# Optimization experiments

Measured on AMD Instinct MI355X. Metric: run time of the kernel, lower is better.

The kernel has to match this reference:

```python
import jax, jax.numpy as jnp
import numpy as np

H = 768      # hidden_size
NH = 12      # num_attention_heads
HD = H // NH # head_dim = 64
EPS = 1e-5


def setup_inputs() -> dict:
    key = jax.random.key(0)
    ks = jax.random.split(key, 12)
    B, S = 2, 2048
    s = 1.0 / np.sqrt(H)
    return {
        "hidden_states": jax.random.normal(ks[0], (B, S, H), dtype=jnp.float32),
        "attention_mask": jax.random.normal(ks[1], (B, S), dtype=jnp.float32),
        "Wq": jax.random.normal(ks[2], (H, H), dtype=jnp.float32) * s,
        "bq": jnp.zeros((H,), dtype=jnp.float32),
        "Wk": jax.random.normal(ks[3], (H, H), dtype=jnp.float32) * s,
        "bk": jnp.zeros((H,), dtype=jnp.float32),
        "Wv": jax.random.normal(ks[4], (H, H), dtype=jnp.float32) * s,
        "bv": jnp.zeros((H,), dtype=jnp.float32),
        "Wo": jax.random.normal(ks[5], (H, H), dtype=jnp.float32) * s,
        "bo": jnp.zeros((H,), dtype=jnp.float32),
        "ln_gamma": jnp.ones((H,), dtype=jnp.float32),
        "ln_beta": jnp.zeros((H,), dtype=jnp.float32),
    }


def reference(hidden_states, attention_mask, Wq, bq, Wk, bk, Wv, bv, Wo, bo, ln_gamma, ln_beta):
    B, S, E = hidden_states.shape
    # QKV projections -> [B, NH, S, HD]
    def proj(W, b):
        return (hidden_states @ W + b).reshape(B, S, NH, HD).transpose(0, 2, 1, 3)
    q = proj(Wq, bq)
    k = proj(Wk, bk)
    v = proj(Wv, bv)
    # scores [B, NH, S, S]
    att = jnp.einsum('bhqd,bhkd->bhqk', q, k) * (1.0 / np.sqrt(HD))
    # padding pair mask: valid iff mask>=0 at both query and key positions
    valid = (attention_mask >= 0)  # [B, S]
    pair = valid[:, None, :, None] & valid[:, None, None, :]  # [B,1,S,S]
    att = jnp.where(pair, att, -1e9)
    att = jax.nn.softmax(att, axis=-1)
    # dropout p=0 (eval) -> identity
    ctx = jnp.einsum('bhqk,bhkd->bhqd', att, v)  # [B,NH,S,HD]
    ctx = ctx.transpose(0, 2, 1, 3).reshape(B, S, E)
    # output dense + residual + LayerNorm
    h = ctx @ Wo + bo + hidden_states
    mu = jnp.mean(h, axis=-1, keepdims=True)
    var = jnp.mean(jnp.square(h - mu), axis=-1, keepdims=True)
    out = (h - mu) * jax.lax.rsqrt(var + EPS) * ln_gamma + ln_beta
    return out
```

## Files before the change

kernel.cpp:

```cpp
#include <hip/hip_runtime.h>
#include <hip/hip_bf16.h>

#define H_DIM 768
#define NHEAD 12
#define HDIM  64
#define S_LEN 2048
#define B_SZ  2
#define M_TOT (B_SZ * S_LEN)
#define NQKV  (3 * H_DIM)
#define LN_EPS 1e-5f
#define SM_C   0.1803368801f

typedef __attribute__((ext_vector_type(8)))  short bf16x8;
typedef __attribute__((ext_vector_type(4)))  float f32x4;
typedef __attribute__((ext_vector_type(16))) float f32x16;
typedef __attribute__((ext_vector_type(4)))  int   i32x4;

static __device__ inline ushort f2bf(float x) {
    __hip_bfloat16 h = __float2bfloat16(x);
    ushort u;
    __builtin_memcpy(&u, &h, 2);
    return u;
}
static __device__ inline float bf2f(ushort u) {
    unsigned int v = ((unsigned int)u) << 16;
    float f;
    __builtin_memcpy(&f, &v, 4);
    return f;
}
static __device__ inline unsigned cvt_pk_bf16(float lo, float hi) {
    unsigned r;
    asm("v_cvt_pk_bf16_f32 %0, %1, %2" : "=v"(r) : "v"(lo), "v"(hi));
    return r;
}

#define GLDS16(g, l) __builtin_amdgcn_global_load_lds( \
    (const __attribute__((address_space(1))) void*)(g), \
    (__attribute__((address_space(3))) void*)(l), 16, 0, 0)

__global__ __launch_bounds__(256)
void prep(const float* __restrict__ hs,
          const float* __restrict__ Wq, const float* __restrict__ Wk,
          const float* __restrict__ Wv, const float* __restrict__ Wo,
          const float* __restrict__ bq, const float* __restrict__ bk,
          const float* __restrict__ bv,
          ushort* __restrict__ Xbf, ushort* __restrict__ Wcat,
          ushort* __restrict__ Wot, float* __restrict__ bcat)
{
    __shared__ ushort T[64][65];
    const int bid = blockIdx.x;
    const int t   = threadIdx.x;

    if (bid < 3072) {
        const int i = (bid * 256 + t) * 4;
        f32x4 v = *(const f32x4*)(hs + i);
        ushort4 o;
        o.x = f2bf(v[0]); o.y = f2bf(v[1]); o.z = f2bf(v[2]); o.w = f2bf(v[3]);
        *(ushort4*)(Xbf + i) = o;
    } else if (bid < 3072 + 576) {
        const int bid2 = bid - 3072;
        const int z = bid2 / 144;
        const int rem = bid2 % 144;
        const int n0 = (rem / 12) * 64;
        const int k0 = (rem % 12) * 64;
        const float* W = (z == 0) ? Wq : (z == 1) ? Wk : (z == 2) ? Wv : Wo;
        const int r = t >> 2, c0 = (t & 3) * 16;
        const float* src = W + (size_t)(k0 + r) * H_DIM + n0 + c0;
        #pragma unroll
        for (int j = 0; j < 16; j += 4) {
            f32x4 v = *(const f32x4*)(src + j);
            #pragma unroll
            for (int jj = 0; jj < 4; ++jj) T[r][c0 + j + jj] = f2bf(v[jj]);
        }
        __syncthreads();
        bf16x8 o0, o1;
        #pragma unroll
        for (int j = 0; j < 8; ++j) {
            o0[j] = (short)T[c0 + j][r];
            o1[j] = (short)T[c0 + 8 + j][r];
        }
        ushort* dst = (z < 3)
            ? Wcat + (size_t)(z * 768 + n0 + r) * H_DIM + k0 + c0
            : Wot  + (size_t)(n0 + r) * H_DIM + k0 + c0;
        *(bf16x8*)dst       = o0;
        *(bf16x8*)(dst + 8) = o1;
    } else {
        const int i = (bid - 3648) * 256 + t;
        if (i < NQKV) {
            float v = (i < 768) ? bq[i] : (i < 1536) ? bk[i - 768] : bv[i - 1536];
            bcat[i] = v;
        }
    }
}

template<int OUTMODE>
__global__ __launch_bounds__(256)
void gemm_mfma(const ushort* __restrict__ A, const ushort* __restrict__ Bt,
               const float* __restrict__ bias, const float* __restrict__ resid,
               void* __restrict__ outp, ushort* __restrict__ vtp,
               int M, int N, int K, int nscale, float sfac)
{
    __shared__ ushort As[128 * 32];
    __shared__ ushort Bs[128 * 32];
    const int bn = blockIdx.x * 128;
    const int bm = blockIdx.y * 128;
    const int t  = threadIdx.x;
    const int w  = t >> 6, l = t & 63;
    const int lg = l >> 4, lr = l & 15;
    const int wr = w >> 1, wc = w & 1;

    f32x4 acc[4][4];
    #pragma unroll
    for (int i = 0; i < 4; ++i)
        #pragma unroll
        for (int j = 0; j < 4; ++j) acc[i][j] = (f32x4){0.f, 0.f, 0.f, 0.f};

    for (int k0 = 0; k0 < K; k0 += 32) {
        #pragma unroll
        for (int it = 0; it < 2; ++it) {
            const int g = it * 256 + t;
            const int r = g >> 2, cb = (g & 3) * 8;
            GLDS16(A  + (size_t)(bm + r) * K + k0 + cb, (char*)As + g * 16);
            GLDS16(Bt + (size_t)(bn + r) * K + k0 + cb, (char*)Bs + g * 16);
        }
        __syncthreads();
        bf16x8 af[4], bfr[4];
        #pragma unroll
        for (int m16 = 0; m16 < 4; ++m16)
            af[m16] = *(const bf16x8*)&As[(wr * 64 + m16 * 16 + lr) * 32 + lg * 8];
        #pragma unroll
        for (int n16 = 0; n16 < 4; ++n16)
            bfr[n16] = *(const bf16x8*)&Bs[(wc * 64 + n16 * 16 + lr) * 32 + lg * 8];
        #pragma unroll
        for (int m16 = 0; m16 < 4; ++m16)
            #pragma unroll
            for (int n16 = 0; n16 < 4; ++n16)
                acc[m16][n16] = __builtin_amdgcn_mfma_f32_16x16x32_bf16(
                    af[m16], bfr[n16], acc[m16][n16], 0, 0, 0);
        __syncthreads();
    }

    #pragma unroll
    for (int m16 = 0; m16 < 4; ++m16) {
        #pragma unroll
        for (int n16 = 0; n16 < 4; ++n16) {
            const int col = bn + wc * 64 + n16 * 16 + lr;
            const float bcol = bias[col];
            const int row0 = bm + wr * 64 + m16 * 16 + lg * 4;
            float vv[4];
            #pragma unroll
            for (int r = 0; r < 4; ++r) {
                float v = acc[m16][n16][r] + bcol;
                if (OUTMODE == 1) v += resid[(size_t)(row0 + r) * N + col];
                else if (col < nscale) v *= sfac;
                vv[r] = v;
            }
            if (OUTMODE == 1) {
                #pragma unroll
                for (int r = 0; r < 4; ++r)
                    ((float*)outp)[(size_t)(row0 + r) * N + col] = vv[r];
            } else if (col >= 1536) {
                const int dfull = col - 1536;
                const int hh = dfull >> 6, dd = dfull & 63;
                const int bb = row0 >> 11, ss = row0 & 2047;
                ushort4 pk;
                pk.x = f2bf(vv[0]); pk.y = f2bf(vv[1]);
                pk.z = f2bf(vv[2]); pk.w = f2bf(vv[3]);
                *(ushort4*)(vtp + ((size_t)(bb * NHEAD + hh) * HDIM + dd) * S_LEN + ss) = pk;
            } else {
                #pragma unroll
                for (int r = 0; r < 4; ++r)
                    ((ushort*)outp)[(size_t)(row0 + r) * N + col] = f2bf(vv[r]);
            }
        }
    }
}

#define KT     64
#define ATT_QT 128
#define KVHALF (S_LEN / 2)
#define NTILES (KVHALF / KT)
#define KMSTR  (KVHALF + 4)

__global__ __launch_bounds__(256, 3)
void attn_mfma(const ushort* __restrict__ Qbf, const ushort* __restrict__ Kbf,
               const ushort* __restrict__ Vt, const float* __restrict__ mask,
               ushort* __restrict__ Pp, float* __restrict__ lp)
{
    const int flat = blockIdx.x;
    const int wk   = (flat & 7) * 96 + (flat >> 3);
    const int qt   = wk & 15;
    const int c_   = wk >> 4;
    const int h    = c_ % 12;
    const int bz   = c_ / 12;
    const int b    = bz >> 1, half = bz & 1;

    const int t  = threadIdx.x;
    const int w  = t >> 6, l = t & 63;
    const int l31 = l & 31, hi = l >> 5;
    const int q0 = qt * ATT_QT;
    const int kb0 = half * KVHALF;

    __shared__ ushort Ks[3][KT][64];
    __shared__ ushort Vs[2][HDIM][64];
    __shared__ float  kmarg[2 * KMSTR];

    {
        const int i = t * 4;
        f32x4 v = *(const f32x4*)(mask + b * S_LEN + kb0 + i);
        f32x4 o;
        #pragma unroll
        for (int j = 0; j < 4; ++j)
            o[j] = (v[j] >= 0.f) ? 0.f : -1e30f;
        *(f32x4*)&kmarg[i] = o;
        *(f32x4*)&kmarg[KMSTR + i] = o;
    }

    const bool qnL = (mask[b * S_LEN + q0 + w * 32 + l31] < 0.f);

    bf16x8 qa[4];
    {
        const ushort* qsrc = Qbf + (size_t)(b * S_LEN + q0 + w * 32 + l31) * NQKV
                           + h * HDIM + 8 * hi;
        #pragma unroll
        for (int k = 0; k < 4; ++k)
            qa[k] = *(const bf16x8*)(qsrc + 16 * k);
    }

    const int u    = l >> 3;
    const int scol = ((l & 7) ^ u) * 8;
    const int srcK = w * 16 + u + ((u & 4) ? 4 : 0);
    const int srow = w * 16 + u;
    const ushort* kLane = Kbf + (size_t)(b * S_LEN + kb0 + srcK) * NQKV
                        + h * HDIM + scol;
    const ushort* vLane = Vt + ((size_t)(b * NHEAD + h) * HDIM + srow) * S_LEN
                        + kb0 + scol;
    char* ldsK = (char*)Ks + w * 2048 + l * 16;
    char* ldsV = (char*)Vs + w * 2048 + l * 16;

    __syncthreads();

    GLDS16(kLane, ldsK);
    GLDS16(kLane + (size_t)4 * NQKV, ldsK + 1024);
    GLDS16(vLane, ldsV);
    GLDS16(vLane + (size_t)8 * S_LEN, ldsV + 1024);
    GLDS16(kLane + (size_t)KT * NQKV, ldsK + 8192);
    GLDS16(kLane + (size_t)(KT + 4) * NQKV, ldsK + 8192 + 1024);

    float l_part = 0.f;
    f32x16 accO[2];
    #pragma unroll
    for (int dt = 0; dt < 2; ++dt)
        #pragma unroll
        for (int i = 0; i < 16; ++i) accO[dt][i] = 0.f;

    const int swzl = (l31 & 7) << 4;
    const float* kmBase = &kmarg[hi * KMSTR];

    for (int tt = 0; tt < NTILES; ++tt) {
        if (tt < NTILES - 1) {
            asm volatile("s_waitcnt vmcnt(2)" ::: "memory");
        } else {
            asm volatile("s_waitcnt vmcnt(0)" ::: "memory");
        }
        __builtin_amdgcn_s_barrier();

        if (tt + 1 < NTILES) {
            const ushort* vsrc = vLane + (size_t)(tt + 1) * KT;
            char* lv = ldsV + ((tt + 1) & 1) * 8192;
            GLDS16(vsrc, lv);
            GLDS16(vsrc + (size_t)8 * S_LEN, lv + 1024);
            if (tt + 2 < NTILES) {
                const ushort* ksrc = kLane + (size_t)(tt + 2) * KT * NQKV;
                char* lk = ldsK + ((tt + 2) % 3) * 8192;
                GLDS16(ksrc, lk);
                GLDS16(ksrc + (size_t)4 * NQKV, lk + 1024);
            }
        }

        const char* Kc = (const char*)Ks + (tt % 3) * 8192;
        const char* Vc = (const char*)Vs + (tt & 1) * 8192;

        #pragma unroll
        for (int kvt = 0; kvt < 2; ++kvt) {
            f32x16 sc;
            __builtin_amdgcn_s_setprio(1);
            {
                const char* abase = Kc + (kvt * 32 + l31) * 128;
                bf16x8 a0 = *(const bf16x8*)(abase + ((16 * hi +  0) ^ swzl));
                bf16x8 a1 = *(const bf16x8*)(abase + ((16 * hi + 32) ^ swzl));
                bf16x8 a2 = *(const bf16x8*)(abase + ((16 * hi + 64) ^ swzl));
                bf16x8 a3 = *(const bf16x8*)(abase + ((16 * hi + 96) ^ swzl));
                f32x16 z;
                #pragma unroll
                for (int i = 0; i < 16; ++i) z[i] = 0.f;
                sc = __builtin_amdgcn_mfma_f32_32x32x16_bf16(a0, qa[0], z, 0, 0, 0);
                sc = __builtin_amdgcn_mfma_f32_32x32x16_bf16(a1, qa[1], sc, 0, 0, 0);
                sc = __builtin_amdgcn_mfma_f32_32x32x16_bf16(a2, qa[2], sc, 0, 0, 0);
                sc = __builtin_amdgcn_mfma_f32_32x32x16_bf16(a3, qa[3], sc, 0, 0, 0);
            }
            __builtin_amdgcn_s_setprio(0);

            float p[16];
            const float* km = kmBase + tt * 64 + kvt * 32;
            #pragma unroll
            for (int q4 = 0; q4 < 4; ++q4) {
                const int kvb = 16 * (q4 >> 1) + 8 * hi + 4 * (q4 & 1);
                f32x4 kq = *(const f32x4*)(km + kvb);
                #pragma unroll
                for (int r = 0; r < 4; ++r) {
                    float arg = sc[q4 * 4 + r] + kq[r];
                    arg = qnL ? 0.f : arg;
                    const float pv = exp2f(arg);
                    p[q4 * 4 + r] = pv;
                    l_part += pv;
                }
            }

            __builtin_amdgcn_s_setprio(1);
            #pragma unroll
            for (int cc = 0; cc < 2; ++cc) {
                i32x4 pku;
                pku[0] = (int)cvt_pk_bf16(p[8 * cc + 0], p[8 * cc + 1]);
                pku[1] = (int)cvt_pk_bf16(p[8 * cc + 2], p[8 * cc + 3]);
                pku[2] = (int)cvt_pk_bf16(p[8 * cc + 4], p[8 * cc + 5]);
                pku[3] = (int)cvt_pk_bf16(p[8 * cc + 6], p[8 * cc + 7]);
                bf16x8 pa;
                __builtin_memcpy(&pa, &pku, 16);
                const int c = kvt * 2 + cc;
                #pragma unroll
                for (int dt = 0; dt < 2; ++dt) {
                    bf16x8 bv = *(const bf16x8*)(Vc + (32 * dt + l31) * 128
                                                 + ((32 * c + 16 * hi) ^ swzl));
                    accO[dt] = __builtin_amdgcn_mfma_f32_32x32x16_bf16(
                        pa, bv, accO[dt], 0, 0, 0);
                }
            }
            __builtin_amdgcn_s_setprio(0);
        }
    }

    l_part += __shfl_xor(l_part, 32, 64);

    const size_t MN = (size_t)M_TOT * H_DIM;
    #pragma unroll
    for (int dt = 0; dt < 2; ++dt) {
        #pragma unroll
        for (int reg = 0; reg < 16; ++reg) {
            const int q = (reg & 3) + 8 * (reg >> 2) + 4 * hi;
            const int m = b * S_LEN + q0 + w * 32 + q;
            Pp[(size_t)half * MN + (size_t)m * H_DIM + h * HDIM + 32 * dt + l31]
                = f2bf(accO[dt][reg]);
        }
    }
    if (hi == 0) {
        const int m = b * S_LEN + q0 + w * 32 + l31;
        lp[half * (M_TOT * NHEAD) + m * NHEAD + h] = l_part;
    }
}

__global__ __launch_bounds__(256)
void combine_kernel(const ushort* __restrict__ Pp, const float* __restrict__ lp,
                    ushort* __restrict__ ctx)
{
    const int idx = blockIdx.x * 256 + threadIdx.x;
    const int m  = idx / 96;
    const int c8 = idx % 96;
    const int c  = c8 * 8;
    const int h  = c8 >> 3;
    const size_t MN = (size_t)M_TOT * H_DIM;

    const float lsum = lp[m * NHEAD + h] + lp[M_TOT * NHEAD + m * NHEAD + h];
    const float inv  = 1.0f / lsum;

    bf16x8 a = *(const bf16x8*)(Pp + (size_t)m * H_DIM + c);
    bf16x8 b = *(const bf16x8*)(Pp + MN + (size_t)m * H_DIM + c);
    bf16x8 o;
    #pragma unroll
    for (int j = 0; j < 8; ++j)
        o[j] = (short)f2bf((bf2f((ushort)a[j]) + bf2f((ushort)b[j])) * inv);
    *(bf16x8*)(ctx + (size_t)m * H_DIM + c) = o;
}

__global__ __launch_bounds__(256)
void ln_kernel(const float* __restrict__ Hbuf, const float* __restrict__ gamma,
               const float* __restrict__ beta, float* __restrict__ out)
{
    const int m = blockIdx.x * 4 + (threadIdx.x >> 6);
    const int l = threadIdx.x & 63;
    const float* row = Hbuf + (size_t)m * H_DIM;

    f32x4 x[3];
    #pragma unroll
    for (int k = 0; k < 3; ++k) x[k] = *(const f32x4*)(row + l * 4 + k * 256);

    float s = 0.f;
    #pragma unroll
    for (int k = 0; k < 3; ++k)
        #pragma unroll
        for (int j = 0; j < 4; ++j) s += x[k][j];
    #pragma unroll
    for (int off = 1; off < 64; off <<= 1) s += __shfl_xor(s, off, 64);
    const float mu = s * (1.0f / H_DIM);

    float v = 0.f;
    #pragma unroll
    for (int k = 0; k < 3; ++k)
        #pragma unroll
        for (int j = 0; j < 4; ++j) {
            const float d = x[k][j] - mu;
            v += d * d;
        }
    #pragma unroll
    for (int off = 1; off < 64; off <<= 1) v += __shfl_xor(v, off, 64);
    const float rstd = rsqrtf(v * (1.0f / H_DIM) + LN_EPS);

    #pragma unroll
    for (int k = 0; k < 3; ++k) {
        const int c = l * 4 + k * 256;
        f32x4 gm = *(const f32x4*)(gamma + c);
        f32x4 bt = *(const f32x4*)(beta + c);
        f32x4 o;
        #pragma unroll
        for (int j = 0; j < 4; ++j)
            o[j] = (x[k][j] - mu) * rstd * gm[j] + bt[j];
        *(f32x4*)(out + (size_t)m * H_DIM + c) = o;
    }
}

extern "C" void kernel_launch(void* const* d_in, const int* in_sizes, int n_in,
                              void* d_out, int out_size, void* d_ws, size_t ws_size,
                              hipStream_t stream)
{
    const float* hs   = (const float*)d_in[0];
    const float* mask = (const float*)d_in[1];
    const float* Wq   = (const float*)d_in[2];
    const float* bq   = (const float*)d_in[3];
    const float* Wk   = (const float*)d_in[4];
    const float* bk   = (const float*)d_in[5];
    const float* Wv   = (const float*)d_in[6];
    const float* bv   = (const float*)d_in[7];
    const float* Wo   = (const float*)d_in[8];
    const float* bo   = (const float*)d_in[9];
    const float* g    = (const float*)d_in[10];
    const float* be   = (const float*)d_in[11];
    float* out = (float*)d_out;

    char* base = (char*)d_ws;
    ushort* Xbf    = (ushort*)(base);
    ushort* QKVbf  = (ushort*)(base + 6291456);
    ushort* Wcat   = (ushort*)(base + 25165824);
    ushort* Wot    = (ushort*)(base + 28704768);
    float*  bcat   = (float*) (base + 29884416);
    ushort* Vt     = (ushort*)(base + 29893632);
    ushort* Cbf    = (ushort*)(base + 36185088);
    float*  Hb     = (float*) (base + 42476544);
    float*  lp     = (float*) (base + 25165824);
    ushort* Pp     = (ushort*)(base + 42476544);

    prep<<<3657, 256, 0, stream>>>(hs, Wq, Wk, Wv, Wo, bq, bk, bv,
                                   Xbf, Wcat, Wot, bcat);

    gemm_mfma<0><<<dim3(NQKV / 128, M_TOT / 128), 256, 0, stream>>>(
        Xbf, Wcat, bcat, nullptr, QKVbf, Vt, M_TOT, NQKV, H_DIM, 768, SM_C);

    attn_mfma<<<768, 256, 0, stream>>>(
        QKVbf, QKVbf + 768, Vt, mask, Pp, lp);

    combine_kernel<<<M_TOT * 96 / 256, 256, 0, stream>>>(Pp, lp, Cbf);

    gemm_mfma<1><<<dim3(H_DIM / 128, M_TOT / 128), 256, 0, stream>>>(
        Cbf, Wot, bo, hs, Hb, nullptr, M_TOT, H_DIM, H_DIM, 0, 1.0f);

    ln_kernel<<<M_TOT / 4, 256, 0, stream>>>(Hb, g, be, out);
}
```

Before: 120.0 us.

## Single-buffer V tile and shrink LDS to fit four attention blocks per CU

```diff
diff --git a/kernel.cpp b/kernel.cpp
--- a/kernel.cpp
+++ b/kernel.cpp
@@ -180,9 +180,8 @@
 #define ATT_QT 128
 #define KVHALF (S_LEN / 2)
 #define NTILES (KVHALF / KT)
-#define KMSTR  (KVHALF + 4)
-
-__global__ __launch_bounds__(256, 3)
+
+__global__ __launch_bounds__(256, 4)
 void attn_mfma(const ushort* __restrict__ Qbf, const ushort* __restrict__ Kbf,
                const ushort* __restrict__ Vt, const float* __restrict__ mask,
                ushort* __restrict__ Pp, float* __restrict__ lp)
@@ -202,8 +201,8 @@
     const int kb0 = half * KVHALF;
 
     __shared__ ushort Ks[3][KT][64];
-    __shared__ ushort Vs[2][HDIM][64];
-    __shared__ float  kmarg[2 * KMSTR];
+    __shared__ ushort Vs[HDIM][64];
+    __shared__ float  kmarg[KVHALF];
 
     {
         const int i = t * 4;
@@ -213,7 +212,6 @@
         for (int j = 0; j < 4; ++j)
             o[j] = (v[j] >= 0.f) ? 0.f : -1e30f;
         *(f32x4*)&kmarg[i] = o;
-        *(f32x4*)&kmarg[KMSTR + i] = o;
     }
 
     const bool qnL = (mask[b * S_LEN + q0 + w * 32 + l31] < 0.f);
@@ -242,10 +240,10 @@
 
     GLDS16(kLane, ldsK);
     GLDS16(kLane + (size_t)4 * NQKV, ldsK + 1024);
-    GLDS16(vLane, ldsV);
-    GLDS16(vLane + (size_t)8 * S_LEN, ldsV + 1024);
     GLDS16(kLane + (size_t)KT * NQKV, ldsK + 8192);
     GLDS16(kLane + (size_t)(KT + 4) * NQKV, ldsK + 8192 + 1024);
+    asm volatile("s_waitcnt vmcnt(2)" ::: "memory");
+    __builtin_amdgcn_s_barrier();
 
     float l_part = 0.f;
     f32x16 accO[2];
@@ -255,32 +253,21 @@
         for (int i = 0; i < 16; ++i) accO[dt][i] = 0.f;
 
     const int swzl = (l31 & 7) << 4;
-    const float* kmBase = &kmarg[hi * KMSTR];
 
     for (int tt = 0; tt < NTILES; ++tt) {
-        if (tt < NTILES - 1) {
-            asm volatile("s_waitcnt vmcnt(2)" ::: "memory");
-        } else {
-            asm volatile("s_waitcnt vmcnt(0)" ::: "memory");
-        }
-        __builtin_amdgcn_s_barrier();
-
-        if (tt + 1 < NTILES) {
-            const ushort* vsrc = vLane + (size_t)(tt + 1) * KT;
-            char* lv = ldsV + ((tt + 1) & 1) * 8192;
-            GLDS16(vsrc, lv);
-            GLDS16(vsrc + (size_t)8 * S_LEN, lv + 1024);
-            if (tt + 2 < NTILES) {
-                const ushort* ksrc = kLane + (size_t)(tt + 2) * KT * NQKV;
-                char* lk = ldsK + ((tt + 2) % 3) * 8192;
-                GLDS16(ksrc, lk);
-                GLDS16(ksrc + (size_t)4 * NQKV, lk + 1024);
-            }
+        const ushort* vsrc = vLane + (size_t)tt * KT;
+        GLDS16(vsrc, ldsV);
+        GLDS16(vsrc + (size_t)8 * S_LEN, ldsV + 1024);
+        if (tt + 2 < NTILES) {
+            const ushort* ksrc = kLane + (size_t)(tt + 2) * KT * NQKV;
+            char* lk = ldsK + ((tt + 2) % 3) * 8192;
+            GLDS16(ksrc, lk);
+            GLDS16(ksrc + (size_t)4 * NQKV, lk + 1024);
         }
 
         const char* Kc = (const char*)Ks + (tt % 3) * 8192;
-        const char* Vc = (const char*)Vs + (tt & 1) * 8192;
-
+
+        i32x4 paq[2][2];
         #pragma unroll
         for (int kvt = 0; kvt < 2; ++kvt) {
             f32x16 sc;
@@ -302,7 +289,7 @@
             __builtin_amdgcn_s_setprio(0);
 
             float p[16];
-            const float* km = kmBase + tt * 64 + kvt * 32;
+            const float* km = &kmarg[tt * 64 + kvt * 32];
             #pragma unroll
             for (int q4 = 0; q4 < 4; ++q4) {
                 const int kvb = 16 * (q4 >> 1) + 8 * hi + 4 * (q4 & 1);
@@ -316,28 +303,43 @@
                     l_part += pv;
                 }
             }
-
-            __builtin_amdgcn_s_setprio(1);
             #pragma unroll
             for (int cc = 0; cc < 2; ++cc) {
-                i32x4 pku;
-                pku[0] = (int)cvt_pk_bf16(p[8 * cc + 0], p[8 * cc + 1]);
-                pku[1] = (int)cvt_pk_bf16(p[8 * cc + 2], p[8 * cc + 3]);
-                pku[2] = (int)cvt_pk_bf16(p[8 * cc + 4], p[8 * cc + 5]);
-                pku[3] = (int)cvt_pk_bf16(p[8 * cc + 6], p[8 * cc + 7]);
+                paq[kvt][cc][0] = (int)cvt_pk_bf16(p[8 * cc + 0], p[8 * cc + 1]);
+                paq[kvt][cc][1] = (int)cvt_pk_bf16(p[8 * cc + 2], p[8 * cc + 3]);
+                paq[kvt][cc][2] = (int)cvt_pk_bf16(p[8 * cc + 4], p[8 * cc + 5]);
+                paq[kvt][cc][3] = (int)cvt_pk_bf16(p[8 * cc + 6], p[8 * cc + 7]);
+            }
+        }
+
+        if (tt + 2 < NTILES) {
+            asm volatile("s_waitcnt vmcnt(2)" ::: "memory");
+        } else {
+            asm volatile("s_waitcnt vmcnt(0)" ::: "memory");
+        }
+        __builtin_amdgcn_s_barrier();
+
+        __builtin_amdgcn_s_setprio(1);
+        #pragma unroll
+        for (int kvt = 0; kvt < 2; ++kvt) {
+            #pragma unroll
+            for (int cc = 0; cc < 2; ++cc) {
                 bf16x8 pa;
-                __builtin_memcpy(&pa, &pku, 16);
+                __builtin_memcpy(&pa, &paq[kvt][cc], 16);
                 const int c = kvt * 2 + cc;
                 #pragma unroll
                 for (int dt = 0; dt < 2; ++dt) {
-                    bf16x8 bv = *(const bf16x8*)(Vc + (32 * dt + l31) * 128
+                    bf16x8 bv = *(const bf16x8*)((const char*)Vs
+                                                 + (32 * dt + l31) * 128
                                                  + ((32 * c + 16 * hi) ^ swzl));
                     accO[dt] = __builtin_amdgcn_mfma_f32_32x32x16_bf16(
                         pa, bv, accO[dt], 0, 0, 0);
                 }
             }
-            __builtin_amdgcn_s_setprio(0);
-        }
+        }
+        __builtin_amdgcn_s_setprio(0);
+
+        __builtin_amdgcn_s_barrier();
     }
 
     l_part += __shfl_xor(l_part, 32, 64);
```

New measurement: 120.2 us. No clear change (+0.1%).

## Fuse split-KV combine into output GEMM and use ballot bitmasks for key mask

Applied to the files above, without the earlier changes.

```diff
diff --git a/kernel.cpp b/kernel.cpp
--- a/kernel.cpp
+++ b/kernel.cpp
@@ -93,12 +93,11 @@
     }
 }
 
-template<int OUTMODE>
 __global__ __launch_bounds__(256)
 void gemm_mfma(const ushort* __restrict__ A, const ushort* __restrict__ Bt,
-               const float* __restrict__ bias, const float* __restrict__ resid,
-               void* __restrict__ outp, ushort* __restrict__ vtp,
-               int M, int N, int K, int nscale, float sfac)
+               const float* __restrict__ bias, void* __restrict__ outp,
+               ushort* __restrict__ vtp, int M, int N, int K,
+               int nscale, float sfac)
 {
     __shared__ ushort As[128 * 32];
     __shared__ ushort Bs[128 * 32];
@@ -151,15 +150,10 @@
             #pragma unroll
             for (int r = 0; r < 4; ++r) {
                 float v = acc[m16][n16][r] + bcol;
-                if (OUTMODE == 1) v += resid[(size_t)(row0 + r) * N + col];
-                else if (col < nscale) v *= sfac;
+                if (col < nscale) v *= sfac;
                 vv[r] = v;
             }
-            if (OUTMODE == 1) {
-                #pragma unroll
-                for (int r = 0; r < 4; ++r)
-                    ((float*)outp)[(size_t)(row0 + r) * N + col] = vv[r];
-            } else if (col >= 1536) {
+            if (col >= 1536) {
                 const int dfull = col - 1536;
                 const int hh = dfull >> 6, dd = dfull & 63;
                 const int bb = row0 >> 11, ss = row0 & 2047;
@@ -176,11 +170,89 @@
     }
 }
 
+__global__ __launch_bounds__(256)
+void gemm_out(const ushort* __restrict__ Pp, const float* __restrict__ lp,
+              const ushort* __restrict__ Bt, const float* __restrict__ bias,
+              const float* __restrict__ resid, float* __restrict__ outp)
+{
+    __shared__ ushort As[128 * 32];
+    __shared__ ushort Bs[128 * 32];
+    const int bn = blockIdx.x * 128;
+    const int bm = blockIdx.y * 128;
+    const int t  = threadIdx.x;
+    const int w  = t >> 6, l = t & 63;
+    const int lg = l >> 4, lr = l & 15;
+    const int wr = w >> 1, wc = w & 1;
+    const size_t MN = (size_t)M_TOT * H_DIM;
+
+    f32x4 acc[4][4];
+    #pragma unroll
+    for (int i = 0; i < 4; ++i)
+        #pragma unroll
+        for (int j = 0; j < 4; ++j) acc[i][j] = (f32x4){0.f, 0.f, 0.f, 0.f};
+
+    for (int k0 = 0; k0 < H_DIM; k0 += 32) {
+        #pragma unroll
+        for (int it = 0; it < 2; ++it) {
+            const int g = it * 256 + t;
+            const int r = g >> 2, cb = (g & 3) * 8;
+            const int m = bm + r;
+            const int c = k0 + cb;
+            const int hh = c >> 6;
+            bf16x8 a0 = *(const bf16x8*)(Pp + (size_t)m * H_DIM + c);
+            bf16x8 a1 = *(const bf16x8*)(Pp + MN + (size_t)m * H_DIM + c);
+            const float inv = 1.0f /
+                (lp[m * NHEAD + hh] + lp[M_TOT * NHEAD + m * NHEAD + hh]);
+            bf16x8 o;
+            #pragma unroll
+            for (int j = 0; j < 8; j += 2) {
+                float x0 = (bf2f((ushort)a0[j])     + bf2f((ushort)a1[j]))     * inv;
+                float x1 = (bf2f((ushort)a0[j + 1]) + bf2f((ushort)a1[j + 1])) * inv;
+                unsigned pk = cvt_pk_bf16(x0, x1);
+                o[j]     = (short)(pk & 0xffff);
+                o[j + 1] = (short)(pk >> 16);
+            }
+            *(bf16x8*)&As[g * 8] = o;
+            GLDS16(Bt + (size_t)(bn + r) * H_DIM + k0 + cb, (char*)Bs + g * 16);
+        }
+        __syncthreads();
+        bf16x8 af[4], bfr[4];
+        #pragma unroll
+        for (int m16 = 0; m16 < 4; ++m16)
+            af[m16] = *(const bf16x8*)&As[(wr * 64 + m16 * 16 + lr) * 32 + lg * 8];
+        #pragma unroll
+        for (int n16 = 0; n16 < 4; ++n16)
+            bfr[n16] = *(const bf16x8*)&Bs[(wc * 64 + n16 * 16 + lr) * 32 + lg * 8];
+        #pragma unroll
+        for (int m16 = 0; m16 < 4; ++m16)
+            #pragma unroll
+            for (int n16 = 0; n16 < 4; ++n16)
+                acc[m16][n16] = __builtin_amdgcn_mfma_f32_16x16x32_bf16(
+                    af[m16], bfr[n16], acc[m16][n16], 0, 0, 0);
+        __syncthreads();
+    }
+
+    #pragma unroll
+    for (int m16 = 0; m16 < 4; ++m16) {
+        #pragma unroll
+        for (int n16 = 0; n16 < 4; ++n16) {
+            const int col = bn + wc * 64 + n16 * 16 + lr;
+            const float bcol = bias[col];
+            const int row0 = bm + wr * 64 + m16 * 16 + lg * 4;
+            #pragma unroll
+            for (int r = 0; r < 4; ++r) {
+                float v = acc[m16][n16][r] + bcol
+                        + resid[(size_t)(row0 + r) * H_DIM + col];
+                outp[(size_t)(row0 + r) * H_DIM + col] = v;
+            }
+        }
+    }
+}
+
 #define KT     64
 #define ATT_QT 128
 #define KVHALF (S_LEN / 2)
 #define NTILES (KVHALF / KT)
-#define KMSTR  (KVHALF + 4)
 
 __global__ __launch_bounds__(256, 3)
 void attn_mfma(const ushort* __restrict__ Qbf, const ushort* __restrict__ Kbf,
@@ -203,18 +275,11 @@
 
     __shared__ ushort Ks[3][KT][64];
     __shared__ ushort Vs[2][HDIM][64];
-    __shared__ float  kmarg[2 * KMSTR];
-
-    {
-        const int i = t * 4;
-        f32x4 v = *(const f32x4*)(mask + b * S_LEN + kb0 + i);
-        f32x4 o;
-        #pragma unroll
-        for (int j = 0; j < 4; ++j)
-            o[j] = (v[j] >= 0.f) ? 0.f : -1e30f;
-        *(f32x4*)&kmarg[i] = o;
-        *(f32x4*)&kmarg[KMSTR + i] = o;
-    }
+
+    unsigned long long kvmsk[NTILES];
+    #pragma unroll
+    for (int tt = 0; tt < NTILES; ++tt)
+        kvmsk[tt] = __ballot(mask[b * S_LEN + kb0 + tt * 64 + l] >= 0.f);
 
     const bool qnL = (mask[b * S_LEN + q0 + w * 32 + l31] < 0.f);
 
@@ -255,8 +320,8 @@
         for (int i = 0; i < 16; ++i) accO[dt][i] = 0.f;
 
     const int swzl = (l31 & 7) << 4;
-    const float* kmBase = &kmarg[hi * KMSTR];
-
+
+    #pragma unroll
     for (int tt = 0; tt < NTILES; ++tt) {
         if (tt < NTILES - 1) {
             asm volatile("s_waitcnt vmcnt(2)" ::: "memory");
@@ -280,6 +345,8 @@
 
         const char* Kc = (const char*)Ks + (tt % 3) * 8192;
         const char* Vc = (const char*)Vs + (tt & 1) * 8192;
+
+        const unsigned long long sh = kvmsk[tt] >> (8 * hi);
 
         #pragma unroll
         for (int kvt = 0; kvt < 2; ++kvt) {
@@ -302,14 +369,13 @@
             __builtin_amdgcn_s_setprio(0);
 
             float p[16];
-            const float* km = kmBase + tt * 64 + kvt * 32;
             #pragma unroll
             for (int q4 = 0; q4 < 4; ++q4) {
-                const int kvb = 16 * (q4 >> 1) + 8 * hi + 4 * (q4 & 1);
-                f32x4 kq = *(const f32x4*)(km + kvb);
                 #pragma unroll
                 for (int r = 0; r < 4; ++r) {
-                    float arg = sc[q4 * 4 + r] + kq[r];
+                    const int bitc = 32 * kvt + 16 * (q4 >> 1) + 4 * (q4 & 1) + r;
+                    const bool kvv = ((unsigned)(sh >> bitc)) & 1u;
+                    float arg = kvv ? sc[q4 * 4 + r] : -1e30f;
                     arg = qnL ? 0.f : arg;
                     const float pv = exp2f(arg);
                     p[q4 * 4 + r] = pv;
@@ -357,29 +423,6 @@
         const int m = b * S_LEN + q0 + w * 32 + l31;
         lp[half * (M_TOT * NHEAD) + m * NHEAD + h] = l_part;
     }
-}
-
-__global__ __launch_bounds__(256)
-void combine_kernel(const ushort* __restrict__ Pp, const float* __restrict__ lp,
-                    ushort* __restrict__ ctx)
-{
-    const int idx = blockIdx.x * 256 + threadIdx.x;
-    const int m  = idx / 96;
-    const int c8 = idx % 96;
-    const int c  = c8 * 8;
-    const int h  = c8 >> 3;
-    const size_t MN = (size_t)M_TOT * H_DIM;
-
-    const float lsum = lp[m * NHEAD + h] + lp[M_TOT * NHEAD + m * NHEAD + h];
-    const float inv  = 1.0f / lsum;
-
-    bf16x8 a = *(const bf16x8*)(Pp + (size_t)m * H_DIM + c);
-    bf16x8 b = *(const bf16x8*)(Pp + MN + (size_t)m * H_DIM + c);
-    bf16x8 o;
-    #pragma unroll
-    for (int j = 0; j < 8; ++j)
-        o[j] = (short)f2bf((bf2f((ushort)a[j]) + bf2f((ushort)b[j])) * inv);
-    *(bf16x8*)(ctx + (size_t)m * H_DIM + c) = o;
 }
 
 __global__ __launch_bounds__(256)
@@ -453,24 +496,21 @@
     ushort* Wot    = (ushort*)(base + 28704768);
     float*  bcat   = (float*) (base + 29884416);
     ushort* Vt     = (ushort*)(base + 29893632);
-    ushort* Cbf    = (ushort*)(base + 36185088);
-    float*  Hb     = (float*) (base + 42476544);
+    float*  Hb     = (float*) (base + 36185088);
     float*  lp     = (float*) (base + 25165824);
-    ushort* Pp     = (ushort*)(base + 42476544);
+    ushort* Pp     = (ushort*)(base + 48768000);
 
     prep<<<3657, 256, 0, stream>>>(hs, Wq, Wk, Wv, Wo, bq, bk, bv,
                                    Xbf, Wcat, Wot, bcat);
 
-    gemm_mfma<0><<<dim3(NQKV / 128, M_TOT / 128), 256, 0, stream>>>(
-        Xbf, Wcat, bcat, nullptr, QKVbf, Vt, M_TOT, NQKV, H_DIM, 768, SM_C);
+    gemm_mfma<<<dim3(NQKV / 128, M_TOT / 128), 256, 0, stream>>>(
+        Xbf, Wcat, bcat, QKVbf, Vt, M_TOT, NQKV, H_DIM, 768, SM_C);
 
     attn_mfma<<<768, 256, 0, stream>>>(
         QKVbf, QKVbf + 768, Vt, mask, Pp, lp);
 
-    combine_kernel<<<M_TOT * 96 / 256, 256, 0, stream>>>(Pp, lp, Cbf);
-
-    gemm_mfma<1><<<dim3(H_DIM / 128, M_TOT / 128), 256, 0, stream>>>(
-        Cbf, Wot, bo, hs, Hb, nullptr, M_TOT, H_DIM, H_DIM, 0, 1.0f);
+    gemm_out<<<dim3(H_DIM / 128, M_TOT / 128), 256, 0, stream>>>(
+        Pp, lp, Wot, bo, hs, Hb);
 
     ln_kernel<<<M_TOT / 4, 256, 0, stream>>>(Hb, g, be, out);
 }
```

New measurement: 131.5 us. 9.6% more time.

## Add dedicated 64x96-tiled output GEMM with bf16 residual buffer and trim mask LDS

Applied to the files above, without the earlier changes.

```diff
diff --git a/kernel.cpp b/kernel.cpp
--- a/kernel.cpp
+++ b/kernel.cpp
@@ -93,12 +93,11 @@
     }
 }
 
-template<int OUTMODE>
 __global__ __launch_bounds__(256)
 void gemm_mfma(const ushort* __restrict__ A, const ushort* __restrict__ Bt,
-               const float* __restrict__ bias, const float* __restrict__ resid,
-               void* __restrict__ outp, ushort* __restrict__ vtp,
-               int M, int N, int K, int nscale, float sfac)
+               const float* __restrict__ bias, void* __restrict__ outp,
+               ushort* __restrict__ vtp, int M, int N, int K,
+               int nscale, float sfac)
 {
     __shared__ ushort As[128 * 32];
     __shared__ ushort Bs[128 * 32];
@@ -151,15 +150,10 @@
             #pragma unroll
             for (int r = 0; r < 4; ++r) {
                 float v = acc[m16][n16][r] + bcol;
-                if (OUTMODE == 1) v += resid[(size_t)(row0 + r) * N + col];
-                else if (col < nscale) v *= sfac;
+                if (col < nscale) v *= sfac;
                 vv[r] = v;
             }
-            if (OUTMODE == 1) {
-                #pragma unroll
-                for (int r = 0; r < 4; ++r)
-                    ((float*)outp)[(size_t)(row0 + r) * N + col] = vv[r];
-            } else if (col >= 1536) {
+            if (col >= 1536) {
                 const int dfull = col - 1536;
                 const int hh = dfull >> 6, dd = dfull & 63;
                 const int bb = row0 >> 11, ss = row0 & 2047;
@@ -176,11 +170,78 @@
     }
 }
 
+__global__ __launch_bounds__(256)
+void gemm_out96(const ushort* __restrict__ A, const ushort* __restrict__ Bt,
+                const float* __restrict__ bias, const float* __restrict__ resid,
+                ushort* __restrict__ outp)
+{
+    __shared__ ushort As[64 * 32];
+    __shared__ ushort Bs[96 * 32];
+    const int bn = blockIdx.x * 96;
+    const int bm = blockIdx.y * 64;
+    const int t  = threadIdx.x;
+    const int w  = t >> 6, l = t & 63;
+    const int lg = l >> 4, lr = l & 15;
+    const int wr = w >> 1, wc = w & 1;
+
+    f32x4 acc[2][3];
+    #pragma unroll
+    for (int i = 0; i < 2; ++i)
+        #pragma unroll
+        for (int j = 0; j < 3; ++j) acc[i][j] = (f32x4){0.f, 0.f, 0.f, 0.f};
+
+    for (int k0 = 0; k0 < H_DIM; k0 += 32) {
+        {
+            const int r = t >> 2, cb = (t & 3) * 8;
+            GLDS16(A + (size_t)(bm + r) * H_DIM + k0 + cb, (char*)As + t * 16);
+        }
+        {
+            const int r = t >> 2, cb = (t & 3) * 8;
+            GLDS16(Bt + (size_t)(bn + r) * H_DIM + k0 + cb, (char*)Bs + t * 16);
+            if (t < 128) {
+                const int g = 256 + t;
+                const int r2 = g >> 2, cb2 = (g & 3) * 8;
+                GLDS16(Bt + (size_t)(bn + r2) * H_DIM + k0 + cb2, (char*)Bs + g * 16);
+            }
+        }
+        __syncthreads();
+        bf16x8 af[2], bfr[3];
+        #pragma unroll
+        for (int m16 = 0; m16 < 2; ++m16)
+            af[m16] = *(const bf16x8*)&As[(wr * 32 + m16 * 16 + lr) * 32 + lg * 8];
+        #pragma unroll
+        for (int n16 = 0; n16 < 3; ++n16)
+            bfr[n16] = *(const bf16x8*)&Bs[(wc * 48 + n16 * 16 + lr) * 32 + lg * 8];
+        #pragma unroll
+        for (int m16 = 0; m16 < 2; ++m16)
+            #pragma unroll
+            for (int n16 = 0; n16 < 3; ++n16)
+                acc[m16][n16] = __builtin_amdgcn_mfma_f32_16x16x32_bf16(
+                    af[m16], bfr[n16], acc[m16][n16], 0, 0, 0);
+        __syncthreads();
+    }
+
+    #pragma unroll
+    for (int m16 = 0; m16 < 2; ++m16) {
+        #pragma unroll
+        for (int n16 = 0; n16 < 3; ++n16) {
+            const int col = bn + wc * 48 + n16 * 16 + lr;
+            const float bcol = bias[col];
+            const int row0 = bm + wr * 32 + m16 * 16 + lg * 4;
+            #pragma unroll
+            for (int r = 0; r < 4; ++r) {
+                float v = acc[m16][n16][r] + bcol
+                        + resid[(size_t)(row0 + r) * H_DIM + col];
+                outp[(size_t)(row0 + r) * H_DIM + col] = f2bf(v);
+            }
+        }
+    }
+}
+
 #define KT     64
 #define ATT_QT 128
 #define KVHALF (S_LEN / 2)
 #define NTILES (KVHALF / KT)
-#define KMSTR  (KVHALF + 4)
 
 __global__ __launch_bounds__(256, 3)
 void attn_mfma(const ushort* __restrict__ Qbf, const ushort* __restrict__ Kbf,
@@ -203,7 +264,7 @@
 
     __shared__ ushort Ks[3][KT][64];
     __shared__ ushort Vs[2][HDIM][64];
-    __shared__ float  kmarg[2 * KMSTR];
+    __shared__ float  kmarg[KVHALF];
 
     {
         const int i = t * 4;
@@ -213,7 +274,6 @@
         for (int j = 0; j < 4; ++j)
             o[j] = (v[j] >= 0.f) ? 0.f : -1e30f;
         *(f32x4*)&kmarg[i] = o;
-        *(f32x4*)&kmarg[KMSTR + i] = o;
     }
 
     const bool qnL = (mask[b * S_LEN + q0 + w * 32 + l31] < 0.f);
@@ -255,7 +315,6 @@
         for (int i = 0; i < 16; ++i) accO[dt][i] = 0.f;
 
     const int swzl = (l31 & 7) << 4;
-    const float* kmBase = &kmarg[hi * KMSTR];
 
     for (int tt = 0; tt < NTILES; ++tt) {
         if (tt < NTILES - 1) {
@@ -302,7 +361,7 @@
             __builtin_amdgcn_s_setprio(0);
 
             float p[16];
-            const float* km = kmBase + tt * 64 + kvt * 32;
+            const float* km = &kmarg[tt * 64 + kvt * 32];
             #pragma unroll
             for (int q4 = 0; q4 < 4; ++q4) {
                 const int kvb = 16 * (q4 >> 1) + 8 * hi + 4 * (q4 & 1);
@@ -383,34 +442,36 @@
 }
 
 __global__ __launch_bounds__(256)
-void ln_kernel(const float* __restrict__ Hbuf, const float* __restrict__ gamma,
+void ln_kernel(const ushort* __restrict__ Hbuf, const float* __restrict__ gamma,
                const float* __restrict__ beta, float* __restrict__ out)
 {
     const int m = blockIdx.x * 4 + (threadIdx.x >> 6);
     const int l = threadIdx.x & 63;
-    const float* row = Hbuf + (size_t)m * H_DIM;
-
-    f32x4 x[3];
-    #pragma unroll
-    for (int k = 0; k < 3; ++k) x[k] = *(const f32x4*)(row + l * 4 + k * 256);
+    const ushort* row = Hbuf + (size_t)m * H_DIM;
+
+    float x[12];
+    #pragma unroll
+    for (int k = 0; k < 3; ++k) {
+        ushort4 v = *(const ushort4*)(row + l * 4 + k * 256);
+        x[k * 4 + 0] = bf2f(v.x);
+        x[k * 4 + 1] = bf2f(v.y);
+        x[k * 4 + 2] = bf2f(v.z);
+        x[k * 4 + 3] = bf2f(v.w);
+    }
 
     float s = 0.f;
     #pragma unroll
-    for (int k = 0; k < 3; ++k)
-        #pragma unroll
-        for (int j = 0; j < 4; ++j) s += x[k][j];
+    for (int j = 0; j < 12; ++j) s += x[j];
     #pragma unroll
     for (int off = 1; off < 64; off <<= 1) s += __shfl_xor(s, off, 64);
     const float mu = s * (1.0f / H_DIM);
 
     float v = 0.f;
     #pragma unroll
-    for (int k = 0; k < 3; ++k)
-        #pragma unroll
-        for (int j = 0; j < 4; ++j) {
-            const float d = x[k][j] - mu;
-            v += d * d;
-        }
+    for (int j = 0; j < 12; ++j) {
+        const float d = x[j] - mu;
+        v += d * d;
+    }
     #pragma unroll
     for (int off = 1; off < 64; off <<= 1) v += __shfl_xor(v, off, 64);
     const float rstd = rsqrtf(v * (1.0f / H_DIM) + LN_EPS);
@@ -423,7 +484,7 @@
         f32x4 o;
         #pragma unroll
         for (int j = 0; j < 4; ++j)
-            o[j] = (x[k][j] - mu) * rstd * gm[j] + bt[j];
+            o[j] = (x[k * 4 + j] - mu) * rstd * gm[j] + bt[j];
         *(f32x4*)(out + (size_t)m * H_DIM + c) = o;
     }
 }
@@ -454,23 +515,23 @@
     float*  bcat   = (float*) (base + 29884416);
     ushort* Vt     = (ushort*)(base + 29893632);
     ushort* Cbf    = (ushort*)(base + 36185088);
-    float*  Hb     = (float*) (base + 42476544);
+    ushort* Pp     = (ushort*)(base + 42476544);
     float*  lp     = (float*) (base + 25165824);
-    ushort* Pp     = (ushort*)(base + 42476544);
+    ushort* Hb2    = Xbf;
 
     prep<<<3657, 256, 0, stream>>>(hs, Wq, Wk, Wv, Wo, bq, bk, bv,
                                    Xbf, Wcat, Wot, bcat);
 
-    gemm_mfma<0><<<dim3(NQKV / 128, M_TOT / 128), 256, 0, stream>>>(
-        Xbf, Wcat, bcat, nullptr, QKVbf, Vt, M_TOT, NQKV, H_DIM, 768, SM_C);
+    gemm_mfma<<<dim3(NQKV / 128, M_TOT / 128), 256, 0, stream>>>(
+        Xbf, Wcat, bcat, QKVbf, Vt, M_TOT, NQKV, H_DIM, 768, SM_C);
 
     attn_mfma<<<768, 256, 0, stream>>>(
         QKVbf, QKVbf + 768, Vt, mask, Pp, lp);
 
     combine_kernel<<<M_TOT * 96 / 256, 256, 0, stream>>>(Pp, lp, Cbf);
 
-    gemm_mfma<1><<<dim3(H_DIM / 128, M_TOT / 128), 256, 0, stream>>>(
-        Cbf, Wot, bo, hs, Hb, nullptr, M_TOT, H_DIM, H_DIM, 0, 1.0f);
-
-    ln_kernel<<<M_TOT / 4, 256, 0, stream>>>(Hb, g, be, out);
-}
+    gemm_out96<<<dim3(H_DIM / 96, M_TOT / 64), 256, 0, stream>>>(
+        Cbf, Wot, bo, hs, Hb2);
+
+    ln_kernel<<<M_TOT / 4, 256, 0, stream>>>(Hb2, g, be, out);
+}
```

Measured after the change: 116.6 us (median of 2 runs). 2.8% less time.
